# Optimization experiments

Hardware: AMD Instinct MI355X
Metric: run time of the kernel (lower is better)

Reference implementation:

```python
import jax, jax.numpy as jnp
import numpy as np

B, N, E = 2, 8192, 131072
IN_C, NF = 4, 32
F_IN = IN_C * NF          # 128, = in_channels * num_features
HID, H, OUT = 64, 8, 64   # hidden_features, nheads, out_features
NEG_SLOPE = 0.2           # GATv2Conv default negative_slope


def setup_inputs() -> dict:
    key = jax.random.key(0)
    ks = jax.random.split(key, 12)
    x = jax.random.normal(ks[0], (B, N, IN_C, NF), dtype=jnp.float32)
    edge_index = jax.random.randint(ks[1], (2, E), 0, N, dtype=jnp.int32)

    def w(k, shape, fan_in):
        return jax.random.normal(k, shape, dtype=jnp.float32) / np.sqrt(fan_in).astype(np.float32)

    # GATv2 layer 1: lin_l (source), lin_r (target), attention vector a, bias
    W1l = w(ks[2], (F_IN, H * HID), F_IN)
    W1r = w(ks[3], (F_IN, H * HID), F_IN)
    att1 = w(ks[4], (H, HID), HID)
    b1 = jnp.zeros((H * HID,), dtype=jnp.float32)
    # GATv2 layer 2: input channels = H*HID = 512
    W2l = w(ks[5], (H * HID, H * OUT), H * HID)
    W2r = w(ks[6], (H * HID, H * OUT), H * HID)
    att2 = w(ks[7], (H, OUT), OUT)
    b2 = jnp.zeros((H * OUT,), dtype=jnp.float32)
    return {"x": x, "edge_index": edge_index,
            "W1l": W1l, "W1r": W1r, "att1": att1, "b1": b1,
            "W2l": W2l, "W2r": W2r, "att2": att2, "b2": b2}


def _gatv2_layer(f, src, dst, Wl, Wr, att, b, heads, ch):
    # f: [N, F_in]; src/dst: [E'] (self-loops included)
    xl = (f @ Wl).reshape(N, heads, ch)   # source-side transform (messages)
    xr = (f @ Wr).reshape(N, heads, ch)   # target-side transform
    e = jax.nn.leaky_relu(xl[src] + xr[dst], NEG_SLOPE)     # [E', H, C]
    logits = jnp.einsum('ehc,hc->eh', e, att)               # [E', H]
    # softmax over incoming edges of each target node
    m = jax.lax.stop_gradient(jax.ops.segment_max(logits, dst, num_segments=N))
    a = jnp.exp(logits - m[dst])
    denom = jax.ops.segment_sum(a, dst, num_segments=N)     # [N, H] (>0: self-loops)
    a = a / denom[dst]
    out = jax.ops.segment_sum(xl[src] * a[:, :, None], dst, num_segments=N)
    return out.reshape(N, heads * ch) + b


def reference(x, edge_index, W1l, W1r, att1, b1, W2l, W2r, att2, b2):
    # add self-loops (PyG GATv2Conv default add_self_loops=True)
    loops = jnp.arange(N, dtype=edge_index.dtype)
    src = jnp.concatenate([edge_index[0], loops])
    dst = jnp.concatenate([edge_index[1], loops])
    feats = x.reshape(B, N, F_IN)  # view(batch, nodes, in_channels*num_features)

    def per_graph(f):
        h = _gatv2_layer(f, src, dst, W1l, W1r, att1, b1, H, HID)   # [N, 512]
        return _gatv2_layer(h, src, dst, W2l, W2r, att2, b2, H, OUT)  # [N, 512]

    h_prime = jax.vmap(per_graph)(feats)   # [B, N, H*OUT]
    return jax.nn.elu(h_prime)             # concat=True branch
```

## Files before the change

### kernel.cpp

```cpp
#include <hip/hip_runtime.h>
#include <cstdint>

#define NN 8192
#define NT 16384
#define EE 131072
#define EPAD (EE + NN)
#define SPAD (EPAD + 3 * NN)
#define FIN 128
#define CH 512
#define NH 8
#define NEG 0.2f

typedef __attribute__((ext_vector_type(8))) short short8;
typedef __attribute__((ext_vector_type(4))) unsigned short u16x4;
typedef __attribute__((ext_vector_type(4))) float f32x4;
typedef __attribute__((ext_vector_type(4))) int i32x4;

__device__ inline unsigned short bf16rne(float x) {
    unsigned u = __float_as_uint(x);
    unsigned r = (u + 0x7FFFu + ((u >> 16) & 1u)) >> 16;
    return (unsigned short)r;
}
__device__ inline float bf16tof(unsigned short h) {
    return __uint_as_float((unsigned)h << 16);
}
__device__ inline void gload16(const void* g, void* l) {
    __builtin_amdgcn_global_load_lds((const __attribute__((address_space(1))) void*)g,
                                     (__attribute__((address_space(3))) void*)l, 16, 0, 0);
}
template <int CTRL>
__device__ inline float dpp_add(float x) {
    int v = __builtin_amdgcn_update_dpp(0, __float_as_int(x), CTRL, 0xF, 0xF, true);
    return x + __int_as_float(v);
}


__global__ __launch_bounds__(256) void k_deg(const int* __restrict__ ei, int* __restrict__ deg) {
    int e = blockIdx.x * 256 + threadIdx.x;
    if (e >= EPAD) return;
    int dst = (e < EE) ? ei[EE + e] : (e - EE);
    atomicAdd(&deg[dst], 1);
}

__global__ __launch_bounds__(1024) void k_scan(const int* __restrict__ deg, int* __restrict__ rowptr) {
    __shared__ int part[1024];
    int t = threadIdx.x;
    int loc[8];
    int s = 0;
#pragma unroll
    for (int i = 0; i < 8; i++) { loc[i] = s; s += (deg[t * 8 + i] + 3) & ~3; }
    part[t] = s;
    __syncthreads();
    if (t == 0) {
        int run = 0;
        for (int i = 0; i < 1024; i++) { int tmp = part[i]; part[i] = run; run += tmp; }
        rowptr[NN] = run;
    }
    __syncthreads();
    int base = part[t];
#pragma unroll
    for (int i = 0; i < 8; i++) rowptr[t * 8 + i] = base + loc[i];
}

__global__ __launch_bounds__(256) void k_scatter(const int* __restrict__ ei, const int* __restrict__ rowptr,
                                                 int* __restrict__ cursor, int* __restrict__ ssrc) {
    int e = blockIdx.x * 256 + threadIdx.x;
    if (e >= EPAD) return;
    int src = (e < EE) ? ei[e] : (e - EE);
    int dst = (e < EE) ? ei[EE + e] : (e - EE);
    int pos = rowptr[dst] + atomicAdd(&cursor[dst], 1);
    ssrc[pos] = src;
}

__global__ __launch_bounds__(256) void k_pad(const int* __restrict__ rowptr, const int* __restrict__ deg,
                                             int* __restrict__ ssrc) {
    int n = blockIdx.x * 256 + threadIdx.x;
    if (n >= NN) return;
    int e = rowptr[n] + deg[n], pe = rowptr[n + 1];
    for (int i = e; i < pe; i++) ssrc[i] = 0;
}


__global__ __launch_bounds__(256) void k_cvt_ah(const float* __restrict__ F,
                                                unsigned short* __restrict__ Ah, int n4) {
    int i = blockIdx.x * 256 + threadIdx.x;
    if (i >= n4) return;
    f32x4 v = ((const f32x4*)F)[i];
#pragma unroll
    for (int c = 0; c < 4; c++) Ah[i * 4 + c] = bf16rne(v[c]);
}

template <int K>
__global__ __launch_bounds__(256) void k_cvt_w(const float* __restrict__ Wl, const float* __restrict__ Wr,
                                               unsigned short* __restrict__ Wh, unsigned short* __restrict__ Wlo) {
    int idx = blockIdx.x * 256 + threadIdx.x;
    int n = idx / K, k = idx % K;
    const float* W = (n < 512) ? Wl : Wr;
    float x = W[k * 512 + (n & 511)];
    unsigned short h = bf16rne(x);
    Wh[idx] = h;
    Wlo[idx] = bf16rne(x - bf16tof(h));
}


template <int K, int USE_BL>
__global__ __launch_bounds__(256) void k_gemm_mfma(const unsigned short* __restrict__ Ah,
                                                   const unsigned short* __restrict__ Bh,
                                                   const unsigned short* __restrict__ Bl,
                                                   unsigned short* __restrict__ XLb,
                                                   float* __restrict__ XR) {
    __shared__ unsigned short sAh[4][128][8], sBh[4][128][8];
    __shared__ unsigned short sBl[USE_BL ? 4 : 1][128][8];
    int tid = threadIdx.x;
    int l = tid & 63;
    int w = tid >> 6, wm = w >> 1, wn = w & 1;
    int m0 = blockIdx.x * 128, n0 = blockIdx.y * 128;
    int lr = l & 15, kh = l >> 4;
    f32x4 acc[4][4] = {};

    for (int k0 = 0; k0 < K; k0 += 32) {
#pragma unroll
        for (int g = 0; g < 2; g++) {
            int cell = g * 256 + tid;
            int ckh = cell >> 7, cr = cell & 127;
            int ka = k0 + ckh * 8;
            gload16(Ah + (size_t)(m0 + cr) * K + ka, &sAh[ckh][cr][0]);
            gload16(Bh + (size_t)(n0 + cr) * K + ka, &sBh[ckh][cr][0]);
            if (USE_BL) gload16(Bl + (size_t)(n0 + cr) * K + ka, &sBl[ckh][cr][0]);
        }
        __syncthreads();
        short8 fah[4], fbh[4], fbl[4];
#pragma unroll
        for (int i = 0; i < 4; i++) {
            fah[i] = *(const short8*)&sAh[kh][wm * 64 + i * 16 + lr][0];
            fbh[i] = *(const short8*)&sBh[kh][wn * 64 + i * 16 + lr][0];
            if (USE_BL) fbl[i] = *(const short8*)&sBl[kh][wn * 64 + i * 16 + lr][0];
        }
#pragma unroll
        for (int i = 0; i < 4; i++)
#pragma unroll
            for (int j = 0; j < 4; j++) {
                if (USE_BL)
                    acc[i][j] = __builtin_amdgcn_mfma_f32_16x16x32_bf16(fah[i], fbl[j], acc[i][j], 0, 0, 0);
                acc[i][j] = __builtin_amdgcn_mfma_f32_16x16x32_bf16(fah[i], fbh[j], acc[i][j], 0, 0, 0);
            }
        __syncthreads();
    }
    int colt = n0 + wn * 64;
    int cb = colt & 511;
    if (colt < 512) {
#pragma unroll
        for (int i = 0; i < 4; i++) {
            int mg = m0 + wm * 64 + i * 16 + kh * 4;
#pragma unroll
            for (int j = 0; j < 4; j++) {
                int cg = cb + j * 16 + lr;
#pragma unroll
                for (int q = 0; q < 4; q++)
                    XLb[(size_t)(mg + q) * CH + cg] = bf16rne(acc[i][j][q]);
            }
        }
    } else {
#pragma unroll
        for (int i = 0; i < 4; i++) {
            int mg = m0 + wm * 64 + i * 16 + kh * 4;
#pragma unroll
            for (int j = 0; j < 4; j++) {
                int cg = cb + j * 16 + lr;
#pragma unroll
                for (int q = 0; q < 4; q++)
                    XR[(size_t)(mg + q) * CH + cg] = acc[i][j][q];
            }
        }
    }
}


#define GATHER(CX, IV)                                                         \
  {                                                                            \
    CX[0] = *(const u16x4*)(XLg + (size_t)IV[0] * CH);                         \
    CX[1] = *(const u16x4*)(XLg + (size_t)IV[1] * CH);                         \
    CX[2] = *(const u16x4*)(XLg + (size_t)IV[2] * CH);                         \
    CX[3] = *(const u16x4*)(XLg + (size_t)IV[3] * CH);                         \
  }

#define PROCESS(CX, cb)                                                        \
  {                                                                            \
    float f[4][4];                                                             \
    _Pragma("unroll") for (int e = 0; e < 4; e++)                              \
      _Pragma("unroll") for (int r = 0; r < 4; r++)                            \
        f[e][r] = bf16tof(CX[e][r]);                                           \
    float z[4];                                                                \
    _Pragma("unroll") for (int e = 0; e < 4; e++) {                            \
      float s = 0.f;                                                           \
      _Pragma("unroll") for (int r = 0; r < 4; r++) {                          \
        float t = f[e][r] + xrv[r];                                            \
        t = fmaxf(t, NEG * t);                                                 \
        s += t * atv[r];                                                       \
      }                                                                        \
      z[e] = s;                                                                \
    }                                                                          \
    _Pragma("unroll") for (int e = 0; e < 4; e++) {                            \
      z[e] = dpp_add<0xB1>(z[e]);                                              \
      z[e] = dpp_add<0x4E>(z[e]);                                              \
      z[e] = dpp_add<0x124>(z[e]);                                             \
      z[e] = dpp_add<0x128>(z[e]);                                             \
    }                                                                          \
    _Pragma("unroll") for (int e = 1; e < 4; e++)                              \
      if ((cb) + e >= end) z[e] = -1e30f;                                      \
    float mc = fmaxf(fmaxf(z[0], z[1]), fmaxf(z[2], z[3]));                    \
    if (__ballot(mc > mh + 8.f) == 0ULL) {                                     \
      float p0 = __expf(z[0] - mh), p1 = __expf(z[1] - mh);                    \
      float p2 = __expf(z[2] - mh), p3 = __expf(z[3] - mh);                    \
      sh += (p0 + p1) + (p2 + p3);                                             \
      _Pragma("unroll") for (int r = 0; r < 4; r++)                            \
        acc[r] += p0 * f[0][r] + p1 * f[1][r] + p2 * f[2][r] + p3 * f[3][r];   \
    } else {                                                                   \
      float nm = fmaxf(mh, mc);                                                \
      float sc = __expf(mh - nm);                                              \
      float p0 = __expf(z[0] - nm), p1 = __expf(z[1] - nm);                    \
      float p2 = __expf(z[2] - nm), p3 = __expf(z[3] - nm);                    \
      sh = sh * sc + (p0 + p1) + (p2 + p3);                                    \
      mh = nm;                                                                 \
      _Pragma("unroll") for (int r = 0; r < 4; r++)                            \
        acc[r] = acc[r] * sc + p0 * f[0][r] + p1 * f[1][r] + p2 * f[2][r] +    \
                 p3 * f[3][r];                                                 \
    }                                                                          \
  }

template <int WRITE_BF16>
__global__ __launch_bounds__(256) void k_node5(const unsigned short* __restrict__ XLb,
                                               const float* __restrict__ XR,
                                               const int* __restrict__ rowptr,
                                               const int* __restrict__ deg,
                                               const int* __restrict__ ssrc,
                                               const float* __restrict__ att,
                                               const float* __restrict__ bias,
                                               float* __restrict__ OUT,
                                               unsigned short* __restrict__ OAh) {
    int w = threadIdx.x >> 6;
    int nid = blockIdx.x * 2 + (w >> 1);
    int g = w & 1;
    int l = threadIdx.x & 63;
    int node = nid & (NN - 1);
    int beg = rowptr[node], pend = rowptr[node + 1];
    int end = beg + deg[node];
    int hb = g * 256 + l * 4;

    const unsigned short* XLg = XLb + (size_t)(nid >> 13) * NN * CH + hb;
    f32x4 xrv = *(const f32x4*)(XR + (size_t)nid * CH + hb);
    f32x4 atv = *(const f32x4*)(att + hb);
    f32x4 acc = {0.f, 0.f, 0.f, 0.f};
    float mh = -1e30f, sh = 0.f;

    i32x4 iA = *(const i32x4*)(ssrc + beg);
    i32x4 iB = iA;
    u16x4 curA[4], curB[4];
    GATHER(curA, iA);
    if (beg + 4 < pend) iB = *(const i32x4*)(ssrc + beg + 4);

    int base = beg;
    while (true) {
        if (base + 4 < pend) GATHER(curB, iB);
        if (base + 8 < pend) iA = *(const i32x4*)(ssrc + base + 8);
        PROCESS(curA, base);
        base += 4;
        if (base >= pend) break;
        if (base + 4 < pend) GATHER(curA, iA);
        if (base + 8 < pend) iB = *(const i32x4*)(ssrc + base + 8);
        PROCESS(curB, base);
        base += 4;
        if (base >= pend) break;
    }

    float inv = 1.f / sh;
    f32x4 biasv = *(const f32x4*)(bias + hb);
    size_t ob = (size_t)nid * CH + hb;
    if (WRITE_BF16) {
        u16x4 hv;
#pragma unroll
        for (int r = 0; r < 4; r++) {
            float wv = acc[r] * inv + biasv[r];
            hv[r] = bf16rne(wv);
        }
        *(u16x4*)(OAh + ob) = hv;
    } else {
        f32x4 ov;
#pragma unroll
        for (int r = 0; r < 4; r++) {
            float wv = acc[r] * inv + biasv[r];
            ov[r] = (wv > 0.f) ? wv : (__expf(wv) - 1.f);
        }
        *(f32x4*)(OUT + ob) = ov;
    }
}


extern "C" void kernel_launch(void* const* d_in, const int* in_sizes, int n_in,
                              void* d_out, int out_size, void* d_ws, size_t ws_size,
                              hipStream_t stream) {
    const float* x    = (const float*)d_in[0];
    const int*   ei   = (const int*)d_in[1];
    const float* W1l  = (const float*)d_in[2];
    const float* W1r  = (const float*)d_in[3];
    const float* att1 = (const float*)d_in[4];
    const float* b1   = (const float*)d_in[5];
    const float* W2l  = (const float*)d_in[6];
    const float* W2r  = (const float*)d_in[7];
    const float* att2 = (const float*)d_in[8];
    const float* b2   = (const float*)d_in[9];
    float* out = (float*)d_out;

    char* ws = (char*)d_ws;
    int* rowptr = (int*)ws;
    int* cursor = rowptr + NN + 1;
    int* deg    = cursor + NN;
    int* ssrc   = deg + NN;
    unsigned short* XLb = (unsigned short*)(((uintptr_t)(ssrc + SPAD) + 255) & ~(uintptr_t)255);
    float* XR = (float*)(XLb + (size_t)NT * CH);
    unsigned short* A_h = (unsigned short*)(XR + (size_t)NT * CH);
    unsigned short* W1h = A_h + (size_t)NT * CH;
    unsigned short* W1o = W1h + 1024 * FIN;
    unsigned short* W2h = W1o + 1024 * FIN;
    unsigned short* W2o = W2h + 1024 * CH;

    hipMemsetAsync(cursor, 0, (size_t)2 * NN * sizeof(int), stream);
    k_deg<<<(EPAD + 255) / 256, 256, 0, stream>>>(ei, deg);
    k_scan<<<1, 1024, 0, stream>>>(deg, rowptr);
    k_scatter<<<(EPAD + 255) / 256, 256, 0, stream>>>(ei, rowptr, cursor, ssrc);
    k_pad<<<NN / 256, 256, 0, stream>>>(rowptr, deg, ssrc);
    k_cvt_w<FIN><<<1024 * FIN / 256, 256, 0, stream>>>(W1l, W1r, W1h, W1o);
    k_cvt_w<CH><<<1024 * CH / 256, 256, 0, stream>>>(W2l, W2r, W2h, W2o);

    k_cvt_ah<<<NT * FIN / 4 / 256, 256, 0, stream>>>(x, A_h, NT * FIN / 4);
    k_gemm_mfma<FIN, 1><<<dim3(NT / 128, 8), 256, 0, stream>>>(A_h, W1h, W1o, XLb, XR);
    k_node5<1><<<NT / 2, 256, 0, stream>>>(XLb, XR, rowptr, deg, ssrc, att1, b1, nullptr, A_h);
    k_gemm_mfma<CH, 0><<<dim3(NT / 128, 8), 256, 0, stream>>>(A_h, W2h, W2o, XLb, XR);
    k_node5<0><<<NT / 2, 256, 0, stream>>>(XLb, XR, rowptr, deg, ssrc, att2, b2, out, nullptr);
}
```

Before: 221.5 us.

## Schedule node-aggregation blocks in descending degree order for load balance

Adds a degree histogram, a reverse scan, and a counting sort that produces a node order with the highest in-degree first. The node aggregation kernels now launch one 128-thread block per (node, graph) pair and take nodes from this order, with the two graphs for the same node placed in adjacent blocks. The aim is to cut tail imbalance from high-degree nodes and to let adjacent blocks share the node's edge list in cache. It adds three small setup kernels and loses the spatial locality of XR and output rows, since blocks no longer follow node index order.

```diff
diff --git a/kernel.cpp b/kernel.cpp
--- a/kernel.cpp
+++ b/kernel.cpp
@@ -78,6 +78,28 @@
     if (n >= NN) return;
     int e = rowptr[n] + deg[n], pe = rowptr[n + 1];
     for (int i = e; i < pe; i++) ssrc[i] = 0;
+}
+
+
+__global__ __launch_bounds__(256) void k_hist(const int* __restrict__ deg, int* __restrict__ hist) {
+    int n = blockIdx.x * 256 + threadIdx.x;
+    if (n >= NN) return;
+    atomicAdd(&hist[min(deg[n], 255)], 1);
+}
+
+__global__ __launch_bounds__(64) void k_binscan(int* __restrict__ hist) {
+    if (threadIdx.x == 0) {
+        int run = 0;
+        for (int b = 255; b >= 0; b--) { int t = hist[b]; hist[b] = run; run += t; }
+    }
+}
+
+__global__ __launch_bounds__(256) void k_order(const int* __restrict__ deg, int* __restrict__ hist,
+                                               int* __restrict__ order) {
+    int n = blockIdx.x * 256 + threadIdx.x;
+    if (n >= NN) return;
+    int pos = atomicAdd(&hist[min(deg[n], 255)], 1);
+    order[pos] = n;
 }
 
 
@@ -229,25 +251,26 @@
   }
 
 template <int WRITE_BF16>
-__global__ __launch_bounds__(256) void k_node5(const unsigned short* __restrict__ XLb,
+__global__ __launch_bounds__(128) void k_node5(const unsigned short* __restrict__ XLb,
                                                const float* __restrict__ XR,
                                                const int* __restrict__ rowptr,
                                                const int* __restrict__ deg,
                                                const int* __restrict__ ssrc,
+                                               const int* __restrict__ order,
                                                const float* __restrict__ att,
                                                const float* __restrict__ bias,
                                                float* __restrict__ OUT,
                                                unsigned short* __restrict__ OAh) {
-    int w = threadIdx.x >> 6;
-    int nid = blockIdx.x * 2 + (w >> 1);
-    int g = w & 1;
+    int g = threadIdx.x >> 6;
     int l = threadIdx.x & 63;
-    int node = nid & (NN - 1);
+    int kb = blockIdx.x;
+    int node = order[kb >> 1];
+    int nid = ((kb & 1) << 13) | node;
     int beg = rowptr[node], pend = rowptr[node + 1];
     int end = beg + deg[node];
     int hb = g * 256 + l * 4;
 
-    const unsigned short* XLg = XLb + (size_t)(nid >> 13) * NN * CH + hb;
+    const unsigned short* XLg = XLb + (size_t)(kb & 1) * NN * CH + hb;
     f32x4 xrv = *(const f32x4*)(XR + (size_t)nid * CH + hb);
     f32x4 atv = *(const f32x4*)(att + hb);
     f32x4 acc = {0.f, 0.f, 0.f, 0.f};
@@ -315,7 +338,9 @@
     int* rowptr = (int*)ws;
     int* cursor = rowptr + NN + 1;
     int* deg    = cursor + NN;
-    int* ssrc   = deg + NN;
+    int* hist   = deg + NN;
+    int* order  = hist + 256;
+    int* ssrc   = order + NN;
     unsigned short* XLb = (unsigned short*)(((uintptr_t)(ssrc + SPAD) + 255) & ~(uintptr_t)255);
     float* XR = (float*)(XLb + (size_t)NT * CH);
     unsigned short* A_h = (unsigned short*)(XR + (size_t)NT * CH);
@@ -324,8 +349,11 @@
     unsigned short* W2h = W1o + 1024 * FIN;
     unsigned short* W2o = W2h + 1024 * CH;
 
-    hipMemsetAsync(cursor, 0, (size_t)2 * NN * sizeof(int), stream);
+    hipMemsetAsync(cursor, 0, (size_t)(2 * NN + 256) * sizeof(int), stream);
     k_deg<<<(EPAD + 255) / 256, 256, 0, stream>>>(ei, deg);
+    k_hist<<<NN / 256, 256, 0, stream>>>(deg, hist);
+    k_binscan<<<1, 64, 0, stream>>>(hist);
+    k_order<<<NN / 256, 256, 0, stream>>>(deg, hist, order);
     k_scan<<<1, 1024, 0, stream>>>(deg, rowptr);
     k_scatter<<<(EPAD + 255) / 256, 256, 0, stream>>>(ei, rowptr, cursor, ssrc);
     k_pad<<<NN / 256, 256, 0, stream>>>(rowptr, deg, ssrc);
@@ -334,7 +362,7 @@
 
     k_cvt_ah<<<NT * FIN / 4 / 256, 256, 0, stream>>>(x, A_h, NT * FIN / 4);
     k_gemm_mfma<FIN, 1><<<dim3(NT / 128, 8), 256, 0, stream>>>(A_h, W1h, W1o, XLb, XR);
-    k_node5<1><<<NT / 2, 256, 0, stream>>>(XLb, XR, rowptr, deg, ssrc, att1, b1, nullptr, A_h);
+    k_node5<1><<<NT, 128, 0, stream>>>(XLb, XR, rowptr, deg, ssrc, order, att1, b1, nullptr, A_h);
     k_gemm_mfma<CH, 0><<<dim3(NT / 128, 8), 256, 0, stream>>>(A_h, W2h, W2o, XLb, XR);
-    k_node5<0><<<NT / 2, 256, 0, stream>>>(XLb, XR, rowptr, deg, ssrc, att2, b2, out, nullptr);
-}
+    k_node5<0><<<NT, 128, 0, stream>>>(XLb, XR, rowptr, deg, ssrc, order, att2, b2, out, nullptr);
+}
```

New measurement: 263.3 us. +18.9%, slower.
